# Kernel tuning notes

Measured on AMD Instinct MI355X. Metric: run time of the kernel, lower is better.

## Reference

```python
import jax, jax.numpy as jnp
import numpy as np


def setup_inputs() -> dict:
    key = jax.random.key(0)
    k1, k2 = jax.random.split(key)
    N = 50000
    E = 800000
    out_features = 64
    edge = jax.random.randint(k1, (2, E), 0, N, dtype=jnp.int64)
    edge_w = jax.random.normal(k2, (E, out_features), dtype=jnp.float32)
    return {"edge": edge, "edge_w": edge_w, "N": N, "E": E, "out_features": out_features}


def reference(edge, edge_w, N, E, out_features):
    # sparse_coo_tensor(edge, edge_w, [N, N, F]) summed over dim=1 reduces to a
    # segment-sum of edge values over the row (source) index edge[0].
    # output[i, f] = sum_{e: edge[0,e]==i} edge_w[e, f]   -> [N, out_features]
    return jax.ops.segment_sum(edge_w, edge[0], num_segments=N)
```

## Files before the change

kernel.cpp:

```cpp
#include <hip/hip_runtime.h>


#define TILE 1024

__global__ __launch_bounds__(256) void hist_kernel(
    const int* __restrict__ edge0, int* __restrict__ counts, int E)
{
    int t = blockIdx.x * blockDim.x + threadIdx.x;
    int base = t * 4;
    if (base + 3 < E) {
        int4 r = ((const int4*)edge0)[t];
        atomicAdd(&counts[r.x], 1);
        atomicAdd(&counts[r.y], 1);
        atomicAdd(&counts[r.z], 1);
        atomicAdd(&counts[r.w], 1);
    } else {
        for (int i = base; i < E; ++i) atomicAdd(&counts[edge0[i]], 1);
    }
}

__global__ __launch_bounds__(256) void scan_partial(
    const int* __restrict__ counts, int* __restrict__ tileSum, int N)
{
    __shared__ int wsum[4];
    int t = threadIdx.x;
    int base = blockIdx.x * TILE + t * 4;
    int s = 0;
    #pragma unroll
    for (int k = 0; k < 4; ++k) {
        int i = base + k;
        if (i < N) s += counts[i];
    }
    for (int off = 1; off < 64; off <<= 1) s += __shfl_xor(s, off);
    if ((t & 63) == 0) wsum[t >> 6] = s;
    __syncthreads();
    if (t == 0) tileSum[blockIdx.x] = wsum[0] + wsum[1] + wsum[2] + wsum[3];
}

__global__ __launch_bounds__(64) void scan_tiles(
    const int* __restrict__ tileSum, int* __restrict__ tileOff, int numTiles,
    int* __restrict__ offsets, int N, int E)
{
    int t = threadIdx.x;
    int v0 = (t < numTiles) ? tileSum[t] : 0;
    int v = v0;
    for (int off = 1; off < 64; off <<= 1) {
        int u = __shfl_up(v, off);
        if (t >= off) v += u;
    }
    if (t < numTiles) tileOff[t] = v - v0;
    if (t == 0) offsets[N] = E;
}

__global__ __launch_bounds__(256) void scan_final(
    const int* __restrict__ counts, const int* __restrict__ tileOff,
    int* __restrict__ offsets, int N)
{
    __shared__ int wtot[4];
    int t = threadIdx.x;
    int lane = t & 63, wv = t >> 6;
    int base = blockIdx.x * TILE + t * 4;
    int c[4]; int s = 0;
    #pragma unroll
    for (int k = 0; k < 4; ++k) {
        int i = base + k;
        c[k] = (i < N) ? counts[i] : 0;
        s += c[k];
    }
    int inc = s;
    for (int off = 1; off < 64; off <<= 1) {
        int u = __shfl_up(inc, off);
        if (lane >= off) inc += u;
    }
    if (lane == 63) wtot[wv] = inc;
    __syncthreads();
    int wpre = 0;
    for (int w = 0; w < wv; ++w) wpre += wtot[w];
    int pre = tileOff[blockIdx.x] + wpre + (inc - s);
    #pragma unroll
    for (int k = 0; k < 4; ++k) {
        int i = base + k;
        if (i < N) offsets[i] = pre;
        pre += c[k];
    }
}

__global__ __launch_bounds__(256) void scatter_kernel(
    const int* __restrict__ edge0, int* __restrict__ cursor,
    int* __restrict__ ids, int E)
{
    int t = blockIdx.x * blockDim.x + threadIdx.x;
    int base = t * 4;
    if (base + 3 < E) {
        int4 r = ((const int4*)edge0)[t];
        ids[atomicAdd(&cursor[r.x], 1)] = base;
        ids[atomicAdd(&cursor[r.y], 1)] = base + 1;
        ids[atomicAdd(&cursor[r.z], 1)] = base + 2;
        ids[atomicAdd(&cursor[r.w], 1)] = base + 3;
    } else {
        for (int i = base; i < E; ++i) ids[atomicAdd(&cursor[edge0[i]], 1)] = i;
    }
}

__global__ __launch_bounds__(256) void reduce_kernel(
    const int* __restrict__ offsets, const int* __restrict__ ids,
    const float4* __restrict__ w4, float4* __restrict__ out4, int N)
{
    int row = blockIdx.x * 4 + (threadIdx.x >> 6);
    if (row >= N) return;
    int lane = threadIdx.x & 63;
    int sub = lane >> 4, q = lane & 15;
    int beg = offsets[row], end = offsets[row + 1];
    float4 acc = make_float4(0.f, 0.f, 0.f, 0.f);
    int j = beg + sub;
    for (; j + 4 < end; j += 8) {
        int e0 = ids[j], e1 = ids[j + 4];
        float4 w0 = w4[(size_t)e0 * 16 + q];
        float4 w1 = w4[(size_t)e1 * 16 + q];
        acc.x += w0.x + w1.x; acc.y += w0.y + w1.y;
        acc.z += w0.z + w1.z; acc.w += w0.w + w1.w;
    }
    if (j < end) {
        int e = ids[j];
        float4 w = w4[(size_t)e * 16 + q];
        acc.x += w.x; acc.y += w.y; acc.z += w.z; acc.w += w.w;
    }
    acc.x += __shfl_xor(acc.x, 16); acc.y += __shfl_xor(acc.y, 16);
    acc.z += __shfl_xor(acc.z, 16); acc.w += __shfl_xor(acc.w, 16);
    acc.x += __shfl_xor(acc.x, 32); acc.y += __shfl_xor(acc.y, 32);
    acc.z += __shfl_xor(acc.z, 32); acc.w += __shfl_xor(acc.w, 32);
    if (sub == 0) out4[(size_t)row * 16 + q] = acc;
}

extern "C" void kernel_launch(void* const* d_in, const int* in_sizes, int n_in,
                              void* d_out, int out_size, void* d_ws, size_t ws_size,
                              hipStream_t stream) {
    const int*   edge   = (const int*)d_in[0];
    const float* edge_w = (const float*)d_in[1];
    int E = in_sizes[0] / 2;
    int N = out_size / 64;
    int numTiles = (N + TILE - 1) / TILE;

    int* counts  = (int*)d_ws;
    int* offsets = counts + N;
    int* cursor  = offsets + N + 1;
    int* ids     = cursor + N;
    int* tileSum = ids + E;
    int* tileOff = tileSum + 64;

    (void)hipMemsetAsync(counts, 0, (size_t)N * sizeof(int), stream);

    int blocksE = (E + 1023) / 1024;
    hist_kernel<<<blocksE, 256, 0, stream>>>(edge, counts, E);
    scan_partial<<<numTiles, 256, 0, stream>>>(counts, tileSum, N);
    scan_tiles<<<1, 64, 0, stream>>>(tileSum, tileOff, numTiles, offsets, N, E);
    scan_final<<<numTiles, 256, 0, stream>>>(counts, tileOff, offsets, N);
    (void)hipMemcpyAsync(cursor, offsets, (size_t)N * sizeof(int),
                         hipMemcpyDeviceToDevice, stream);
    scatter_kernel<<<blocksE, 256, 0, stream>>>(edge, cursor, ids, E);

    int blocksR = (N + 3) / 4;
    reduce_kernel<<<blocksR, 256, 0, stream>>>(offsets, ids, (const float4*)edge_w,
                                               (float4*)d_out, N);
}
```

Measured before the change: 386.2 us.

## Record atomic ranks in histogram, use single-block scan, drop cursor atomics

The histogram kernel now stores the value each atomicAdd returns as a per-edge rank, so the scatter pass computes each destination as offsets[row]+rank with no atomics and no cursor copy. The three-kernel tiled scan is replaced by one 1024-thread block in which each thread sums a contiguous strip serially. The reduce loop gains a 16-stride unrolled stage with four outstanding gathers per lane. This removes two launches, a device memcpy and the scatter atomics, at the cost of an extra rank array write and read and a single-block scan that walks the counts serially per thread.

New measurement: 422.6 us. 9.5% more time.

```diff
diff --git a/kernel.cpp b/kernel.cpp
--- a/kernel.cpp
+++ b/kernel.cpp
@@ -1,72 +1,36 @@
 #include <hip/hip_runtime.h>
 
 
-#define TILE 1024
-
-__global__ __launch_bounds__(256) void hist_kernel(
-    const int* __restrict__ edge0, int* __restrict__ counts, int E)
+__global__ __launch_bounds__(256) void hist_rank_kernel(
+    const int* __restrict__ edge0, int* __restrict__ counts,
+    int* __restrict__ rank, int E)
 {
     int t = blockIdx.x * blockDim.x + threadIdx.x;
     int base = t * 4;
     if (base + 3 < E) {
         int4 r = ((const int4*)edge0)[t];
-        atomicAdd(&counts[r.x], 1);
-        atomicAdd(&counts[r.y], 1);
-        atomicAdd(&counts[r.z], 1);
-        atomicAdd(&counts[r.w], 1);
+        int4 k;
+        k.x = atomicAdd(&counts[r.x], 1);
+        k.y = atomicAdd(&counts[r.y], 1);
+        k.z = atomicAdd(&counts[r.z], 1);
+        k.w = atomicAdd(&counts[r.w], 1);
+        ((int4*)rank)[t] = k;
     } else {
-        for (int i = base; i < E; ++i) atomicAdd(&counts[edge0[i]], 1);
+        for (int i = base; i < E; ++i) rank[i] = atomicAdd(&counts[edge0[i]], 1);
     }
 }
 
-__global__ __launch_bounds__(256) void scan_partial(
-    const int* __restrict__ counts, int* __restrict__ tileSum, int N)
+__global__ __launch_bounds__(1024) void scan_kernel(
+    const int* __restrict__ counts, int* __restrict__ offsets, int N, int E)
 {
-    __shared__ int wsum[4];
+    __shared__ int wtot[16];
     int t = threadIdx.x;
-    int base = blockIdx.x * TILE + t * 4;
+    int per = (N + 1023) / 1024;
+    int b0 = t * per;
+    int b1 = min(N, b0 + per);
     int s = 0;
-    #pragma unroll
-    for (int k = 0; k < 4; ++k) {
-        int i = base + k;
-        if (i < N) s += counts[i];
-    }
-    for (int off = 1; off < 64; off <<= 1) s += __shfl_xor(s, off);
-    if ((t & 63) == 0) wsum[t >> 6] = s;
-    __syncthreads();
-    if (t == 0) tileSum[blockIdx.x] = wsum[0] + wsum[1] + wsum[2] + wsum[3];
-}
-
-__global__ __launch_bounds__(64) void scan_tiles(
-    const int* __restrict__ tileSum, int* __restrict__ tileOff, int numTiles,
-    int* __restrict__ offsets, int N, int E)
-{
-    int t = threadIdx.x;
-    int v0 = (t < numTiles) ? tileSum[t] : 0;
-    int v = v0;
-    for (int off = 1; off < 64; off <<= 1) {
-        int u = __shfl_up(v, off);
-        if (t >= off) v += u;
-    }
-    if (t < numTiles) tileOff[t] = v - v0;
-    if (t == 0) offsets[N] = E;
-}
-
-__global__ __launch_bounds__(256) void scan_final(
-    const int* __restrict__ counts, const int* __restrict__ tileOff,
-    int* __restrict__ offsets, int N)
-{
-    __shared__ int wtot[4];
-    int t = threadIdx.x;
+    for (int i = b0; i < b1; ++i) s += counts[i];
     int lane = t & 63, wv = t >> 6;
-    int base = blockIdx.x * TILE + t * 4;
-    int c[4]; int s = 0;
-    #pragma unroll
-    for (int k = 0; k < 4; ++k) {
-        int i = base + k;
-        c[k] = (i < N) ? counts[i] : 0;
-        s += c[k];
-    }
     int inc = s;
     for (int off = 1; off < 64; off <<= 1) {
         int u = __shfl_up(inc, off);
@@ -76,29 +40,26 @@
     __syncthreads();
     int wpre = 0;
     for (int w = 0; w < wv; ++w) wpre += wtot[w];
-    int pre = tileOff[blockIdx.x] + wpre + (inc - s);
-    #pragma unroll
-    for (int k = 0; k < 4; ++k) {
-        int i = base + k;
-        if (i < N) offsets[i] = pre;
-        pre += c[k];
-    }
+    int pre = wpre + (inc - s);
+    for (int i = b0; i < b1; ++i) { offsets[i] = pre; pre += counts[i]; }
+    if (t == 0) offsets[N] = E;
 }
 
 __global__ __launch_bounds__(256) void scatter_kernel(
-    const int* __restrict__ edge0, int* __restrict__ cursor,
-    int* __restrict__ ids, int E)
+    const int* __restrict__ edge0, const int* __restrict__ rank,
+    const int* __restrict__ offsets, int* __restrict__ ids, int E)
 {
     int t = blockIdx.x * blockDim.x + threadIdx.x;
     int base = t * 4;
     if (base + 3 < E) {
         int4 r = ((const int4*)edge0)[t];
-        ids[atomicAdd(&cursor[r.x], 1)] = base;
-        ids[atomicAdd(&cursor[r.y], 1)] = base + 1;
-        ids[atomicAdd(&cursor[r.z], 1)] = base + 2;
-        ids[atomicAdd(&cursor[r.w], 1)] = base + 3;
+        int4 k = ((const int4*)rank)[t];
+        ids[offsets[r.x] + k.x] = base;
+        ids[offsets[r.y] + k.y] = base + 1;
+        ids[offsets[r.z] + k.z] = base + 2;
+        ids[offsets[r.w] + k.w] = base + 3;
     } else {
-        for (int i = base; i < E; ++i) ids[atomicAdd(&cursor[edge0[i]], 1)] = i;
+        for (int i = base; i < E; ++i) ids[offsets[edge0[i]] + rank[i]] = i;
     }
 }
 
@@ -113,6 +74,17 @@
     int beg = offsets[row], end = offsets[row + 1];
     float4 acc = make_float4(0.f, 0.f, 0.f, 0.f);
     int j = beg + sub;
+    for (; j + 12 < end; j += 16) {
+        int e0 = ids[j], e1 = ids[j + 4], e2 = ids[j + 8], e3 = ids[j + 12];
+        float4 w0 = w4[(size_t)e0 * 16 + q];
+        float4 w1 = w4[(size_t)e1 * 16 + q];
+        float4 w2 = w4[(size_t)e2 * 16 + q];
+        float4 w3 = w4[(size_t)e3 * 16 + q];
+        acc.x += (w0.x + w1.x) + (w2.x + w3.x);
+        acc.y += (w0.y + w1.y) + (w2.y + w3.y);
+        acc.z += (w0.z + w1.z) + (w2.z + w3.z);
+        acc.w += (w0.w + w1.w) + (w2.w + w3.w);
+    }
     for (; j + 4 < end; j += 8) {
         int e0 = ids[j], e1 = ids[j + 4];
         float4 w0 = w4[(size_t)e0 * 16 + q];
@@ -139,25 +111,18 @@
     const float* edge_w = (const float*)d_in[1];
     int E = in_sizes[0] / 2;
     int N = out_size / 64;
-    int numTiles = (N + TILE - 1) / TILE;
 
     int* counts  = (int*)d_ws;
     int* offsets = counts + N;
-    int* cursor  = offsets + N + 1;
-    int* ids     = cursor + N;
-    int* tileSum = ids + E;
-    int* tileOff = tileSum + 64;
+    int* rank    = offsets + N + 1;
+    int* ids     = rank + E;
 
     (void)hipMemsetAsync(counts, 0, (size_t)N * sizeof(int), stream);
 
     int blocksE = (E + 1023) / 1024;
-    hist_kernel<<<blocksE, 256, 0, stream>>>(edge, counts, E);
-    scan_partial<<<numTiles, 256, 0, stream>>>(counts, tileSum, N);
-    scan_tiles<<<1, 64, 0, stream>>>(tileSum, tileOff, numTiles, offsets, N, E);
-    scan_final<<<numTiles, 256, 0, stream>>>(counts, tileOff, offsets, N);
-    (void)hipMemcpyAsync(cursor, offsets, (size_t)N * sizeof(int),
-                         hipMemcpyDeviceToDevice, stream);
-    scatter_kernel<<<blocksE, 256, 0, stream>>>(edge, cursor, ids, E);
+    hist_rank_kernel<<<blocksE, 256, 0, stream>>>(edge, counts, rank, E);
+    scan_kernel<<<1, 1024, 0, stream>>>(counts, offsets, N, E);
+    scatter_kernel<<<blocksE, 256, 0, stream>>>(edge, rank, offsets, ids, E);
 
     int blocksR = (N + 3) / 4;
     reduce_kernel<<<blocksR, 256, 0, stream>>>(offsets, ids, (const float4*)edge_w,
```

## Record atomic ranks in histogram pass and batch 16 rows per reduce block

Applied to the files above, without the earlier changes.

The histogram kernel now saves the value returned by each atomic increment as a per-edge rank. The scatter pass then writes ids at offsets[row]+rank with no atomics, and the cursor copy is dropped. The reduce kernel now has each block handle 16 consecutive rows, sharing the block's edge range across all threads. It finds each edge's row by binary search over shared offsets and accumulates with shared-memory float atomics. This aims to balance uneven row lengths and remove contended global atomics, at the cost of an extra rank array, shared-atomic contention, and nondeterministic float summation order.

Result: slower. 549.7 us (+42.4%).

```diff
diff --git a/kernel.cpp b/kernel.cpp
--- a/kernel.cpp
+++ b/kernel.cpp
@@ -3,19 +3,22 @@
 
 #define TILE 1024
 
-__global__ __launch_bounds__(256) void hist_kernel(
-    const int* __restrict__ edge0, int* __restrict__ counts, int E)
+__global__ __launch_bounds__(256) void hist_rank_kernel(
+    const int* __restrict__ edge0, int* __restrict__ counts,
+    int* __restrict__ rank, int E)
 {
     int t = blockIdx.x * blockDim.x + threadIdx.x;
     int base = t * 4;
     if (base + 3 < E) {
         int4 r = ((const int4*)edge0)[t];
-        atomicAdd(&counts[r.x], 1);
-        atomicAdd(&counts[r.y], 1);
-        atomicAdd(&counts[r.z], 1);
-        atomicAdd(&counts[r.w], 1);
+        int4 k;
+        k.x = atomicAdd(&counts[r.x], 1);
+        k.y = atomicAdd(&counts[r.y], 1);
+        k.z = atomicAdd(&counts[r.z], 1);
+        k.w = atomicAdd(&counts[r.w], 1);
+        ((int4*)rank)[t] = k;
     } else {
-        for (int i = base; i < E; ++i) atomicAdd(&counts[edge0[i]], 1);
+        for (int i = base; i < E; ++i) rank[i] = atomicAdd(&counts[edge0[i]], 1);
     }
 }
 
@@ -86,19 +89,20 @@
 }
 
 __global__ __launch_bounds__(256) void scatter_kernel(
-    const int* __restrict__ edge0, int* __restrict__ cursor,
-    int* __restrict__ ids, int E)
+    const int* __restrict__ edge0, const int* __restrict__ rank,
+    const int* __restrict__ offsets, int* __restrict__ ids, int E)
 {
     int t = blockIdx.x * blockDim.x + threadIdx.x;
     int base = t * 4;
     if (base + 3 < E) {
         int4 r = ((const int4*)edge0)[t];
-        ids[atomicAdd(&cursor[r.x], 1)] = base;
-        ids[atomicAdd(&cursor[r.y], 1)] = base + 1;
-        ids[atomicAdd(&cursor[r.z], 1)] = base + 2;
-        ids[atomicAdd(&cursor[r.w], 1)] = base + 3;
+        int4 k = ((const int4*)rank)[t];
+        ids[offsets[r.x] + k.x] = base;
+        ids[offsets[r.y] + k.y] = base + 1;
+        ids[offsets[r.z] + k.z] = base + 2;
+        ids[offsets[r.w] + k.w] = base + 3;
     } else {
-        for (int i = base; i < E; ++i) ids[atomicAdd(&cursor[edge0[i]], 1)] = i;
+        for (int i = base; i < E; ++i) ids[offsets[edge0[i]] + rank[i]] = i;
     }
 }
 
@@ -106,30 +110,34 @@
     const int* __restrict__ offsets, const int* __restrict__ ids,
     const float4* __restrict__ w4, float4* __restrict__ out4, int N)
 {
-    int row = blockIdx.x * 4 + (threadIdx.x >> 6);
-    if (row >= N) return;
-    int lane = threadIdx.x & 63;
-    int sub = lane >> 4, q = lane & 15;
-    int beg = offsets[row], end = offsets[row + 1];
-    float4 acc = make_float4(0.f, 0.f, 0.f, 0.f);
-    int j = beg + sub;
-    for (; j + 4 < end; j += 8) {
-        int e0 = ids[j], e1 = ids[j + 4];
-        float4 w0 = w4[(size_t)e0 * 16 + q];
-        float4 w1 = w4[(size_t)e1 * 16 + q];
-        acc.x += w0.x + w1.x; acc.y += w0.y + w1.y;
-        acc.z += w0.z + w1.z; acc.w += w0.w + w1.w;
-    }
-    if (j < end) {
+    __shared__ float acc[16][64];
+    __shared__ int offs[17];
+    int t = threadIdx.x;
+    int r0 = blockIdx.x * 16;
+    int rlim = min(16, N - r0);
+    if (t < 17) offs[t] = offsets[r0 + (t < rlim ? t : rlim)];
+    ((float4*)acc)[t] = make_float4(0.f, 0.f, 0.f, 0.f);
+    __syncthreads();
+
+    int beg = offs[0], end = offs[16];
+    int slot = t >> 4, q = t & 15;
+    for (int j = beg + slot; j < end; j += 16) {
         int e = ids[j];
         float4 w = w4[(size_t)e * 16 + q];
-        acc.x += w.x; acc.y += w.y; acc.z += w.z; acc.w += w.w;
+        int row = 0;
+        if (offs[row + 8] <= j) row += 8;
+        if (offs[row + 4] <= j) row += 4;
+        if (offs[row + 2] <= j) row += 2;
+        if (offs[row + 1] <= j) row += 1;
+        float* a = &acc[row][q * 4];
+        atomicAdd(a + 0, w.x);
+        atomicAdd(a + 1, w.y);
+        atomicAdd(a + 2, w.z);
+        atomicAdd(a + 3, w.w);
     }
-    acc.x += __shfl_xor(acc.x, 16); acc.y += __shfl_xor(acc.y, 16);
-    acc.z += __shfl_xor(acc.z, 16); acc.w += __shfl_xor(acc.w, 16);
-    acc.x += __shfl_xor(acc.x, 32); acc.y += __shfl_xor(acc.y, 32);
-    acc.z += __shfl_xor(acc.z, 32); acc.w += __shfl_xor(acc.w, 32);
-    if (sub == 0) out4[(size_t)row * 16 + q] = acc;
+    __syncthreads();
+    if (slot < rlim)
+        out4[(size_t)(r0 + slot) * 16 + q] = *(const float4*)&acc[slot][q * 4];
 }
 
 extern "C" void kernel_launch(void* const* d_in, const int* in_sizes, int n_in,
@@ -143,23 +151,21 @@
 
     int* counts  = (int*)d_ws;
     int* offsets = counts + N;
-    int* cursor  = offsets + N + 1;
-    int* ids     = cursor + N;
+    int* rank    = offsets + N + 1;
+    int* ids     = rank + E;
     int* tileSum = ids + E;
     int* tileOff = tileSum + 64;
 
     (void)hipMemsetAsync(counts, 0, (size_t)N * sizeof(int), stream);
 
     int blocksE = (E + 1023) / 1024;
-    hist_kernel<<<blocksE, 256, 0, stream>>>(edge, counts, E);
+    hist_rank_kernel<<<blocksE, 256, 0, stream>>>(edge, counts, rank, E);
     scan_partial<<<numTiles, 256, 0, stream>>>(counts, tileSum, N);
     scan_tiles<<<1, 64, 0, stream>>>(tileSum, tileOff, numTiles, offsets, N, E);
     scan_final<<<numTiles, 256, 0, stream>>>(counts, tileOff, offsets, N);
-    (void)hipMemcpyAsync(cursor, offsets, (size_t)N * sizeof(int),
-                         hipMemcpyDeviceToDevice, stream);
-    scatter_kernel<<<blocksE, 256, 0, stream>>>(edge, cursor, ids, E);
+    scatter_kernel<<<blocksE, 256, 0, stream>>>(edge, rank, offsets, ids, E);
 
-    int blocksR = (N + 3) / 4;
+    int blocksR = (N + 15) / 16;
     reduce_kernel<<<blocksR, 256, 0, stream>>>(offsets, ids, (const float4*)edge_w,
                                                (float4*)d_out, N);
 }
```
